# Performance work log

Measured on AMD Instinct MI355X. Metric: run time of the kernel, lower is better.

The kernel has to match this reference:

```python
import jax, jax.numpy as jnp
import numpy as np

N_FREQS = 10
EPS = 1e-5

def embed(p):
    # NeRF positional embedding: [p, sin(p*2^0), cos(p*2^0), ..., sin(p*2^9), cos(p*2^9)]
    freqs = 2.0 ** jnp.arange(N_FREQS, dtype=p.dtype)  # [10]
    ang = p[:, :, None] * freqs[None, None, :]          # [N,3,10]
    sc = jnp.stack([jnp.sin(ang), jnp.cos(ang)], axis=-1)  # [N,3,10,2]
    return jnp.concatenate([p, sc.reshape(p.shape[0], -1)], axis=-1)  # [N, 63]

def edge_conv(x, edge_index, w1, b1, w2, b2):
    src, dst = edge_index[0], edge_index[1]
    xi = x[dst]                                # target features [E, F]
    h = jnp.concatenate([xi, x[src] - xi], -1)  # [E, 2F]
    h = jax.nn.relu(h @ w1 + b1) @ w2 + b2      # [E, out]
    n = x.shape[0]
    s = jax.ops.segment_sum(h, dst, num_segments=n)
    cnt = jax.ops.segment_sum(jnp.ones((h.shape[0],), h.dtype), dst, num_segments=n)
    return s / jnp.clip(cnt, 1.0)[:, None]      # mean aggregation

def batch_norm(x, gamma, beta):
    mu = jnp.mean(x, axis=0)
    var = jnp.mean((x - mu) ** 2, axis=0)
    return (x - mu) * jax.lax.rsqrt(var + EPS) * gamma + beta

def distribute_features(features, face_indices, num_vertices):
    n, f = features.shape
    feat = features.reshape(n * 3, f // 3)
    idx = face_indices.reshape(-1)
    vsum = jax.ops.segment_sum(feat, idx, num_segments=num_vertices)
    cnt = jax.ops.segment_sum(jnp.ones((idx.shape[0],), feat.dtype), idx, num_segments=num_vertices)
    vmean = vsum / jnp.clip(cnt, 1.0)[:, None]
    return vmean[idx].reshape(n, f)

def _mlp_params(key, in_dim, out_dim):
    k1, k2, k3, k4 = jax.random.split(key, 4)
    h = 2 * out_dim
    return (jax.random.normal(k1, (2 * in_dim, h), jnp.float32) * (1.0 / np.sqrt(2 * in_dim)),
            jax.random.normal(k2, (h,), jnp.float32) * 0.01,
            jax.random.normal(k3, (h, out_dim), jnp.float32) * (1.0 / np.sqrt(h)),
            jax.random.normal(k4, (out_dim,), jnp.float32) * 0.01)

def setup_inputs() -> dict:
    key = jax.random.key(0)
    ks = jax.random.split(key, 10)
    N, E, V = 100000, 300000, 50000
    inp = {
        'x': jax.random.normal(ks[0], (N, 16), jnp.float32),
        'edge_index': jax.random.randint(ks[1], (2, E), 0, N, jnp.int32),
        'faces': jax.random.randint(ks[2], (N, 3), 0, V, jnp.int32),
        'num_vertices': V,
    }
    dims = [(196, 96), (96, 192), (192, 384), (384, 384), (384, 576)]
    for i, (di, do) in enumerate(dims, start=1):
        w1, b1, w2, b2 = _mlp_params(ks[2 + i], di, do)
        inp[f'gc{i}_w1'], inp[f'gc{i}_b1'], inp[f'gc{i}_w2'], inp[f'gc{i}_b2'] = w1, b1, w2, b2
    for i, d in enumerate([96, 192, 384, 384], start=1):
        inp[f'gamma{i}'] = jnp.ones((d,), jnp.float32)
        inp[f'beta{i}'] = jnp.zeros((d,), jnp.float32)
    return inp

def reference(x, edge_index, faces, num_vertices,
              gc1_w1, gc1_b1, gc1_w2, gc1_b2,
              gc2_w1, gc2_b1, gc2_w2, gc2_b2,
              gc3_w1, gc3_b1, gc3_w2, gc3_b2,
              gc4_w1, gc4_b1, gc4_w2, gc4_b2,
              gc5_w1, gc5_b1, gc5_w2, gc5_b2,
              gamma1, beta1, gamma2, beta2, gamma3, beta3, gamma4, beta4):
    h = jnp.concatenate([embed(x[:, :3]), embed(x[:, 3:6]), embed(x[:, 6:9]), x[:, 9:]], -1)  # [N,196]
    h = jax.nn.relu(batch_norm(edge_conv(h, edge_index, gc1_w1, gc1_b1, gc1_w2, gc1_b2), gamma1, beta1))
    h = distribute_features(h, faces, num_vertices)
    h = jax.nn.relu(batch_norm(edge_conv(h, edge_index, gc2_w1, gc2_b1, gc2_w2, gc2_b2), gamma2, beta2))
    h = distribute_features(h, faces, num_vertices)
    h = jax.nn.relu(batch_norm(edge_conv(h, edge_index, gc3_w1, gc3_b1, gc3_w2, gc3_b2), gamma3, beta3))
    h = distribute_features(h, faces, num_vertices)
    h = jax.nn.relu(batch_norm(edge_conv(h, edge_index, gc4_w1, gc4_b1, gc4_w2, gc4_b2), gamma4, beta4))
    h = distribute_features(h, faces, num_vertices)
    h = edge_conv(h, edge_index, gc5_w1, gc5_b1, gc5_w2, gc5_b2)
    h = distribute_features(h, faces, num_vertices)
    return h
```

## Files before the change

kernel.cpp:

```cpp
#include <hip/hip_runtime.h>
#include <hip/hip_bf16.h>
#include <stdint.h>


typedef __hip_bfloat16 bf16;
typedef __attribute__((ext_vector_type(8))) short bf16x8;
typedef __attribute__((ext_vector_type(4))) float f32x4;
#define CHUNK 384

static inline int cdiv(int a, int b) { return (a + b - 1) / b; }

__device__ __forceinline__ float bf2f(bf16 v) { return __bfloat162float(v); }
__device__ __forceinline__ bf16 f2bf(float v) { return __float2bfloat16(v); }
__device__ __forceinline__ unsigned short f2bs(float v) {
  bf16 h = __float2bfloat16(v);
  return *reinterpret_cast<unsigned short*>(&h);
}

__device__ __forceinline__ void gload16(const bf16* g, bf16* lds_base) {
  __builtin_amdgcn_global_load_lds((const __attribute__((address_space(1))) void*)g,
                                   (__attribute__((address_space(3))) void*)lds_base,
                                   16, 0, 0);
}

#define WAIT_VM0 asm volatile("s_waitcnt vmcnt(0)" ::: "memory")

__device__ __forceinline__ void swz_decode(int T, int nn, int& mb, int& nb) {
  int i = blockIdx.x;
  int q = T >> 3, r = T & 7;
  int xcd = i & 7, rank = i >> 3;
  int wg = (xcd < r ? xcd * (q + 1) : r * (q + 1) + (xcd - r) * q) + rank;
  nb = wg % nn;
  mb = wg / nn;
}

__global__ __launch_bounds__(256) void k_embed(const float* __restrict__ x,
                                               bf16* __restrict__ h, int N) {
  int idx = blockIdx.x * 256 + threadIdx.x;
  if (idx >= N * 224) return;
  int n = idx / 224;
  int c = idx - n * 224;
  float v = 0.f;
  if (c >= 196) {
    v = 0.f;
  } else if (c >= 189) {
    v = x[n * 16 + 9 + (c - 189)];
  } else {
    int g = c / 63;
    int cc = c - g * 63;
    const float* p = x + n * 16 + g * 3;
    if (cc < 3) {
      v = p[cc];
    } else {
      int t = cc - 3;
      int comp = t / 20;
      int rem = t - comp * 20;
      float ang = p[comp] * (float)(1 << (rem >> 1));
      v = (rem & 1) ? cosf(ang) : sinf(ang);
    }
  }
  h[idx] = f2bf(v);
}

__global__ __launch_bounds__(256) void k_count(const int* __restrict__ idxs,
                                               int* __restrict__ deg, int M) {
  int i = blockIdx.x * 256 + threadIdx.x;
  if (i < M) atomicAdd(&deg[idxs[i]], 1);
}

__global__ __launch_bounds__(256) void k_recip(const int* __restrict__ deg,
                                               float* __restrict__ r, int n) {
  int i = blockIdx.x * 256 + threadIdx.x;
  if (i < n) {
    int d = deg[i];
    r[i] = d > 0 ? 1.f / (float)d : 0.f;
  }
}

__global__ __launch_bounds__(1024) void k_scan(const int* __restrict__ deg,
                                               int* __restrict__ off,
                                               int* __restrict__ cursor, int n) {
  __shared__ int part[1024];
  int t = threadIdx.x;
  int per = (n + 1023) / 1024;
  int b = t * per;
  int e = b + per;
  if (b > n) b = n;
  if (e > n) e = n;
  int s = 0;
  for (int i = b; i < e; ++i) s += deg[i];
  part[t] = s;
  __syncthreads();
  if (t == 0) {
    int r = 0;
    for (int i = 0; i < 1024; ++i) {
      int x = part[i];
      part[i] = r;
      r += x;
    }
    off[n] = r;
  }
  __syncthreads();
  int r = part[t];
  for (int i = b; i < e; ++i) {
    off[i] = r;
    cursor[i] = r;
    r += deg[i];
  }
}

__global__ __launch_bounds__(256) void k_fill_edges(const int* __restrict__ ei, int E,
                                                    int* __restrict__ cursor,
                                                    int* __restrict__ esrc) {
  int e = blockIdx.x * 256 + threadIdx.x;
  if (e >= E) return;
  int dst = ei[E + e];
  int pos = atomicAdd(&cursor[dst], 1);
  esrc[pos] = ei[e];
}

__global__ __launch_bounds__(256) void k_fill_faces(const int* __restrict__ faces, int M,
                                                    int* __restrict__ cursor,
                                                    int* __restrict__ vidx) {
  int i = blockIdx.x * 256 + threadIdx.x;
  if (i >= M) return;
  int v = faces[i];
  int pos = atomicAdd(&cursor[v], 1);
  vidx[pos] = i;
}

__global__ __launch_bounds__(256) void k_prep_w1(const float* __restrict__ w1,
                                                 bf16* __restrict__ WdT,
                                                 bf16* __restrict__ WbT,
                                                 int F, int H, int F_pad, int H_pad) {
  int idx = blockIdx.x * 256 + threadIdx.x;
  if (idx >= H_pad * F_pad) return;
  int n = idx / F_pad;
  int k = idx - n * F_pad;
  float vd = 0.f, vb = 0.f;
  if (n < H && k < F) {
    float top = w1[(size_t)k * H + n];
    float bot = w1[(size_t)(F + k) * H + n];
    vd = top - bot;
    vb = bot;
  }
  WdT[idx] = f2bf(vd);
  WbT[idx] = f2bf(vb);
}

__global__ __launch_bounds__(256) void k_prep_w2(const float* __restrict__ w2,
                                                 bf16* __restrict__ W2T, int H, int O,
                                                 int O_pad) {
  int idx = blockIdx.x * 256 + threadIdx.x;
  if (idx >= O_pad * H) return;
  int n = idx / H;
  int k = idx - n * H;
  float v = (n < O) ? w2[(size_t)k * O + n] : 0.f;
  W2T[idx] = f2bf(v);
}

__global__ __launch_bounds__(256) void gemm1_mfma(
    const bf16* __restrict__ A, int lda,
    const bf16* __restrict__ WdT, const bf16* __restrict__ WbT,
    const float* __restrict__ b1, int c0,
    bf16* __restrict__ outC, bf16* __restrict__ outB,
    int N, int K_pad, int Hc, int nn) {
  __shared__ bf16 sA[2][128 * 32];
  __shared__ bf16 sBd[2][128 * 32];
  __shared__ bf16 sBb[2][128 * 32];
  int mb, nb;
  swz_decode(gridDim.x, nn, mb, nb);
  const int tid = threadIdx.x;
  const int lane = tid & 63, wv = tid >> 6;
  const int wm = wv & 1, wn = wv >> 1;
  const int lr = lane & 15, quad = lane >> 4;
  const int m_blk = mb * 128, n_blk = nb * 128;
  const int rs = lane >> 2;
  const int cg = (lane & 3) ^ ((lane >> 3) & 3);
  const int gsw = (quad ^ ((lr >> 1) & 3)) << 3;
  f32x4 accC[4][4], accB[4][4];
#pragma unroll
  for (int i = 0; i < 4; ++i)
#pragma unroll
    for (int j = 0; j < 4; ++j) {
      accC[i][j] = (f32x4){0.f, 0.f, 0.f, 0.f};
      accB[i][j] = (f32x4){0.f, 0.f, 0.f, 0.f};
    }

  auto stage = [&](int kt, int buf) {
    const int k0 = (kt << 5) + cg * 8;
#pragma unroll
    for (int i = 0; i < 2; ++i) {
      const int rb = wv * 32 + i * 16;
      const int ro = rb + rs;
      gload16(A + (size_t)(m_blk + ro) * lda + k0, &sA[buf][rb * 32]);
      gload16(WdT + (size_t)(n_blk + ro) * K_pad + k0, &sBd[buf][rb * 32]);
      gload16(WbT + (size_t)(n_blk + ro) * K_pad + k0, &sBb[buf][rb * 32]);
    }
  };
  auto compute = [&](int buf) {
    bf16x8 af[4];
#pragma unroll
    for (int im = 0; im < 4; ++im)
      af[im] = *(const bf16x8*)&sA[buf][(wm * 64 + im * 16 + lr) * 32 + gsw];
#pragma unroll
    for (int jn = 0; jn < 4; ++jn) {
      int go = (wn * 64 + jn * 16 + lr) * 32 + gsw;
      bf16x8 bd = *(const bf16x8*)&sBd[buf][go];
      bf16x8 bb = *(const bf16x8*)&sBb[buf][go];
#pragma unroll
      for (int im = 0; im < 4; ++im) {
        accC[im][jn] = __builtin_amdgcn_mfma_f32_16x16x32_bf16(af[im], bd, accC[im][jn], 0, 0, 0);
        accB[im][jn] = __builtin_amdgcn_mfma_f32_16x16x32_bf16(af[im], bb, accB[im][jn], 0, 0, 0);
      }
    }
  };

  const int kTiles = K_pad >> 5;
  stage(0, 0);
  WAIT_VM0;
  __builtin_amdgcn_s_barrier();
  int cur = 0;
  for (int kt = 0; kt < kTiles - 1; ++kt) {
    stage(kt + 1, cur ^ 1);
    compute(cur);
    WAIT_VM0;
    __builtin_amdgcn_s_barrier();
    cur ^= 1;
  }
  compute(cur);

#pragma unroll
  for (int jn = 0; jn < 4; ++jn) {
    int c = n_blk + wn * 64 + jn * 16 + lr;
    if (c >= Hc) continue;
    float bv = b1[c0 + c];
#pragma unroll
    for (int im = 0; im < 4; ++im) {
      int mb2 = m_blk + wm * 64 + im * 16 + quad * 4;
#pragma unroll
      for (int rg = 0; rg < 4; ++rg) {
        int r = mb2 + rg;
        if (r >= N) continue;
        size_t o = (size_t)r * Hc + c;
        outC[o] = f2bf(accC[im][jn][rg] + bv);
        outB[o] = f2bf(accB[im][jn][rg]);
      }
    }
  }
}

__global__ __launch_bounds__(256) void gemm2_mfma(
    const bf16* __restrict__ S, int ldS,
    const bf16* __restrict__ W2T, int ldw,
    const float* __restrict__ b2, const float* __restrict__ rdeg,
    float* __restrict__ Eo, float* __restrict__ stats, int do_stats,
    int N, int K, int O, int nn) {
  __shared__ bf16 sA[2][128 * 32];
  __shared__ bf16 sB[2][128 * 32];
  int mb, nb;
  swz_decode(gridDim.x, nn, mb, nb);
  const int tid = threadIdx.x;
  const int lane = tid & 63, wv = tid >> 6;
  const int wm = wv & 1, wn = wv >> 1;
  const int lr = lane & 15, quad = lane >> 4;
  const int m_blk = mb * 128, n_blk = nb * 128;
  const int rs = lane >> 2;
  const int cg = (lane & 3) ^ ((lane >> 3) & 3);
  const int gsw = (quad ^ ((lr >> 1) & 3)) << 3;
  f32x4 acc[4][4];
#pragma unroll
  for (int i = 0; i < 4; ++i)
#pragma unroll
    for (int j = 0; j < 4; ++j) acc[i][j] = (f32x4){0.f, 0.f, 0.f, 0.f};

  auto stage = [&](int kt, int buf) {
    const int k0 = (kt << 5) + cg * 8;
#pragma unroll
    for (int i = 0; i < 2; ++i) {
      const int rb = wv * 32 + i * 16;
      const int ro = rb + rs;
      gload16(S + (size_t)(m_blk + ro) * ldS + k0, &sA[buf][rb * 32]);
      gload16(W2T + (size_t)(n_blk + ro) * ldw + k0, &sB[buf][rb * 32]);
    }
  };
  auto compute = [&](int buf) {
    bf16x8 af[4];
#pragma unroll
    for (int im = 0; im < 4; ++im)
      af[im] = *(const bf16x8*)&sA[buf][(wm * 64 + im * 16 + lr) * 32 + gsw];
#pragma unroll
    for (int jn = 0; jn < 4; ++jn) {
      bf16x8 bb = *(const bf16x8*)&sB[buf][(wn * 64 + jn * 16 + lr) * 32 + gsw];
#pragma unroll
      for (int im = 0; im < 4; ++im)
        acc[im][jn] = __builtin_amdgcn_mfma_f32_16x16x32_bf16(af[im], bb, acc[im][jn], 0, 0, 0);
    }
  };

  const int kTiles = K >> 5;
  stage(0, 0);
  WAIT_VM0;
  __builtin_amdgcn_s_barrier();
  int cur = 0;
  for (int kt = 0; kt < kTiles - 1; ++kt) {
    stage(kt + 1, cur ^ 1);
    compute(cur);
    WAIT_VM0;
    __builtin_amdgcn_s_barrier();
    cur ^= 1;
  }
  compute(cur);

  float rdv[4][4];
#pragma unroll
  for (int im = 0; im < 4; ++im) {
    int mb2 = m_blk + wm * 64 + im * 16 + quad * 4;
#pragma unroll
    for (int rg = 0; rg < 4; ++rg) {
      int r = mb2 + rg;
      rdv[im][rg] = (r < N) ? rdeg[r] : 0.f;
    }
  }
#pragma unroll
  for (int jn = 0; jn < 4; ++jn) {
    int c = n_blk + wn * 64 + jn * 16 + lr;
    if (c >= O) continue;
    float b2v = b2[c];
    float ssum = 0.f, qsum = 0.f;
#pragma unroll
    for (int im = 0; im < 4; ++im) {
      int mb2 = m_blk + wm * 64 + im * 16 + quad * 4;
#pragma unroll
      for (int rg = 0; rg < 4; ++rg) {
        int r = mb2 + rg;
        if (r >= N) continue;
        float rd = rdv[im][rg];
        float v = acc[im][jn][rg] * rd;
        if (rd != 0.f) v += b2v;
        Eo[(size_t)r * O + c] = v;
        ssum += v;
        qsum += v * v;
      }
    }
    if (do_stats) {
      ssum += __shfl_xor(ssum, 16);
      ssum += __shfl_xor(ssum, 32);
      qsum += __shfl_xor(qsum, 16);
      qsum += __shfl_xor(qsum, 32);
      if (quad == 0) {
        unsafeAtomicAdd(&stats[c], ssum);
        unsafeAtomicAdd(&stats[O + c], qsum);
      }
    }
  }
}

__global__ __launch_bounds__(256) void k_edge_gather(
    const int* __restrict__ eoff, const int* __restrict__ esrc,
    const bf16* __restrict__ C, const bf16* __restrict__ B,
    bf16* __restrict__ S, int ldS, int c0, int N, int Hc) {
  int gw = (blockIdx.x * 256 + threadIdx.x) >> 6;
  int lane = threadIdx.x & 63;
  if (gw >= N) return;
  int beg = eoff[gw], end = eoff[gw + 1];
  const uint32_t* Crow = reinterpret_cast<const uint32_t*>(C + (size_t)gw * Hc);
  float cc0[3], cc1[3], acc0[3], acc1[3];
#pragma unroll
  for (int w = 0; w < 3; ++w) {
    acc0[w] = 0.f;
    acc1[w] = 0.f;
    cc0[w] = 0.f;
    cc1[w] = 0.f;
    int j2 = lane + w * 64;
    if (j2 * 2 < Hc) {
      uint32_t uc = Crow[j2];
      cc0[w] = __uint_as_float(uc << 16);
      cc1[w] = __uint_as_float(uc & 0xffff0000u);
    }
  }
  for (int e = beg; e < end; ++e) {
    int src = esrc[e];
    const uint32_t* Brow = reinterpret_cast<const uint32_t*>(B + (size_t)src * Hc);
#pragma unroll
    for (int w = 0; w < 3; ++w) {
      int j2 = lane + w * 64;
      if (j2 * 2 < Hc) {
        uint32_t ub = Brow[j2];
        acc0[w] += fmaxf(cc0[w] + __uint_as_float(ub << 16), 0.f);
        acc1[w] += fmaxf(cc1[w] + __uint_as_float(ub & 0xffff0000u), 0.f);
      }
    }
  }
  uint32_t* Srow = reinterpret_cast<uint32_t*>(S + (size_t)gw * ldS + c0);
#pragma unroll
  for (int w = 0; w < 3; ++w) {
    int j2 = lane + w * 64;
    if (j2 * 2 < Hc)
      Srow[j2] = ((uint32_t)f2bs(acc1[w]) << 16) | (uint32_t)f2bs(acc0[w]);
  }
}

__global__ __launch_bounds__(256) void k_bn_finalize(const float* __restrict__ stats,
                                                     const float* __restrict__ gamma,
                                                     const float* __restrict__ beta,
                                                     float* __restrict__ scale,
                                                     float* __restrict__ shift, int N, int O) {
  int c = blockIdx.x * 256 + threadIdx.x;
  if (c >= O) return;
  float mu = stats[c] / (float)N;
  float var = stats[O + c] / (float)N - mu * mu;
  float sc = gamma[c] * rsqrtf(var + 1e-5f);
  scale[c] = sc;
  shift[c] = beta[c] - mu * sc;
}

__global__ __launch_bounds__(256) void k_vgather(
    const int* __restrict__ voff, const int* __restrict__ vidx,
    const float* __restrict__ Ef, const float* __restrict__ scale,
    const float* __restrict__ shift, int use_bn,
    float* __restrict__ Vf, int V, int O, int O3) {
  int idx = blockIdx.x * 256 + threadIdx.x;
  if (idx >= V * O3) return;
  int v = idx / O3;
  int c = idx - v * O3;
  int beg = voff[v], end = voff[v + 1];
  float acc = 0.f;
  for (int e = beg; e < end; ++e) {
    int i = vidx[e];
    int n = i / 3;
    int g = i - n * 3;
    int col = g * O3 + c;
    float x = Ef[(size_t)n * O + col];
    if (use_bn) x = fmaxf(fmaf(x, scale[col], shift[col]), 0.f);
    acc += x;
  }
  Vf[idx] = acc;
}

__global__ __launch_bounds__(256) void k_gather_bf16(const float* __restrict__ Vf,
                                                     const int* __restrict__ faces,
                                                     const float* __restrict__ rv,
                                                     bf16* __restrict__ out,
                                                     int N, int O, int O3) {
  int idx = blockIdx.x * 256 + threadIdx.x;
  if (idx >= N * O) return;
  int n = idx / O;
  int c = idx - n * O;
  int g = c / O3;
  int vert = faces[n * 3 + g];
  out[idx] = f2bf(Vf[(size_t)vert * O3 + (c - g * O3)] * rv[vert]);
}

__global__ __launch_bounds__(256) void k_gather_f32(const float* __restrict__ Vf,
                                                    const int* __restrict__ faces,
                                                    const float* __restrict__ rv,
                                                    float* __restrict__ out,
                                                    int N, int O, int O3) {
  int idx = blockIdx.x * 256 + threadIdx.x;
  if (idx >= N * O) return;
  int n = idx / O;
  int c = idx - n * O;
  int g = c / O3;
  int vert = faces[n * 3 + g];
  out[idx] = Vf[(size_t)vert * O3 + (c - g * O3)] * rv[vert];
}

extern "C" void kernel_launch(void* const* d_in, const int* in_sizes, int n_in,
                              void* d_out, int out_size, void* d_ws, size_t ws_size,
                              hipStream_t stream) {
  (void)n_in; (void)out_size; (void)ws_size;
  const float* x = (const float*)d_in[0];
  const int* ei = (const int*)d_in[1];
  const int* faces = (const int*)d_in[2];
  const int N = in_sizes[0] / 16;
  const int E = in_sizes[1] / 2;
  const int V = 50000;
  const int N_pad = cdiv(N, 128) * 128;

  char* p = (char*)d_ws;
  auto carve = [&](size_t bytes) -> char* {
    char* r = p;
    p += (bytes + 255) & ~(size_t)255;
    return r;
  };
  bf16* buf_h = (bf16*)carve((size_t)N_pad * 384 * sizeof(bf16));
  float* buf_e = (float*)carve((size_t)N * 384 * sizeof(float));
  bf16* buf_C = (bf16*)carve((size_t)N * CHUNK * sizeof(bf16));
  bf16* buf_B = (bf16*)carve((size_t)N * CHUNK * sizeof(bf16));
  bf16* buf_S = (bf16*)carve((size_t)N_pad * 1152 * sizeof(bf16));
  float* buf_V = (float*)carve((size_t)V * 192 * sizeof(float));
  bf16* buf_WdT = (bf16*)carve((size_t)1050000 * sizeof(bf16));
  bf16* buf_WbT = (bf16*)carve((size_t)1050000 * sizeof(bf16));
  bf16* buf_W2T = (bf16*)carve((size_t)1500000 * sizeof(bf16));
  int* ideg = (int*)carve((size_t)N * 4);
  int* ivdeg = (int*)carve((size_t)V * 4);
  float* rdegN = (float*)carve((size_t)N * 4);
  float* rdegV = (float*)carve((size_t)V * 4);
  float* stats = (float*)carve(2 * 576 * 4);
  float* scale = (float*)carve(576 * 4);
  float* shift = (float*)carve(576 * 4);
  int* e_off = (int*)carve((size_t)(N + 1) * 4);
  int* e_cur = (int*)carve((size_t)N * 4);
  int* e_src = (int*)carve((size_t)E * 4);
  int* v_off = (int*)carve((size_t)(V + 1) * 4);
  int* v_cur = (int*)carve((size_t)V * 4);
  int* v_idx = (int*)carve((size_t)3 * N * 4);

  hipMemsetAsync(ideg, 0, (size_t)N * 4, stream);
  hipMemsetAsync(ivdeg, 0, (size_t)V * 4, stream);
  k_count<<<cdiv(E, 256), 256, 0, stream>>>(ei + E, ideg, E);
  k_count<<<cdiv(3 * N, 256), 256, 0, stream>>>(faces, ivdeg, 3 * N);
  k_recip<<<cdiv(N, 256), 256, 0, stream>>>(ideg, rdegN, N);
  k_recip<<<cdiv(V, 256), 256, 0, stream>>>(ivdeg, rdegV, V);

  k_scan<<<1, 1024, 0, stream>>>(ideg, e_off, e_cur, N);
  k_scan<<<1, 1024, 0, stream>>>(ivdeg, v_off, v_cur, V);
  k_fill_edges<<<cdiv(E, 256), 256, 0, stream>>>(ei, E, e_cur, e_src);
  k_fill_faces<<<cdiv(3 * N, 256), 256, 0, stream>>>(faces, 3 * N, v_cur, v_idx);

  k_embed<<<cdiv(N * 224, 256), 256, 0, stream>>>(x, buf_h, N);

  const int LF[5] = {196, 96, 192, 384, 384};
  const int LH[5] = {192, 384, 768, 768, 1152};
  const int LO[5] = {96, 192, 384, 384, 576};

  size_t off1 = 0, off2 = 0;
  const int nm = cdiv(N, 128);

  for (int l = 0; l < 5; ++l) {
    const int F = LF[l], H = LH[l], O = LO[l], O3 = O / 3;
    const int F_pad = ((F + 31) / 32) * 32;
    int Hc_last = H % CHUNK;
    if (Hc_last == 0) Hc_last = CHUNK;
    const int H_pad = H - Hc_last + cdiv(Hc_last, 128) * 128;
    const int O_pad = cdiv(O, 128) * 128;
    const float* w1 = (const float*)d_in[4 + l * 4];
    const float* b1 = (const float*)d_in[5 + l * 4];
    const float* w2 = (const float*)d_in[6 + l * 4];
    const float* b2 = (const float*)d_in[7 + l * 4];
    float* Ebuf = (l == 4) ? (float*)d_out : buf_e;
    bf16* WdT = buf_WdT + off1;
    bf16* WbT = buf_WbT + off1;
    bf16* W2T = buf_W2T + off2;
    off1 += (size_t)H_pad * F_pad;
    off2 += (size_t)O_pad * H;

    k_prep_w1<<<cdiv(H_pad * F_pad, 256), 256, 0, stream>>>(w1, WdT, WbT, F, H, F_pad, H_pad);
    k_prep_w2<<<cdiv(O_pad * H, 256), 256, 0, stream>>>(w2, W2T, H, O, O_pad);

    for (int c0 = 0; c0 < H; c0 += CHUNK) {
      int Hc = (H - c0 < CHUNK) ? (H - c0) : CHUNK;
      int nn1 = cdiv(Hc, 128);
      gemm1_mfma<<<nm * nn1, 256, 0, stream>>>(buf_h, F_pad,
                                               WdT + (size_t)c0 * F_pad, WbT + (size_t)c0 * F_pad,
                                               b1, c0, buf_C, buf_B, N, F_pad, Hc, nn1);
      k_edge_gather<<<cdiv(N * 64, 256), 256, 0, stream>>>(e_off, e_src, buf_C, buf_B,
                                                           buf_S, H, c0, N, Hc);
    }

    if (l < 4) hipMemsetAsync(stats, 0, (size_t)2 * O * 4, stream);
    int nn2 = cdiv(O, 128);
    gemm2_mfma<<<nm * nn2, 256, 0, stream>>>(buf_S, H, W2T, H, b2, rdegN, Ebuf,
                                             stats, (l < 4) ? 1 : 0, N, H, O, nn2);

    if (l < 4)
      k_bn_finalize<<<cdiv(O, 256), 256, 0, stream>>>(
          stats, (const float*)d_in[24 + l * 2], (const float*)d_in[25 + l * 2],
          scale, shift, N, O);

    k_vgather<<<cdiv(V * O3, 256), 256, 0, stream>>>(v_off, v_idx, Ebuf, scale, shift,
                                                     (l < 4) ? 1 : 0, buf_V, V, O, O3);
    if (l < 4)
      k_gather_bf16<<<cdiv(N * O, 256), 256, 0, stream>>>(buf_V, faces, rdegV, buf_h, N, O, O3);
    else
      k_gather_f32<<<cdiv(N * O, 256), 256, 0, stream>>>(buf_V, faces, rdegV, (float*)d_out, N, O, O3);
  }
}
```

Before: 4.542 ms.

## Deepen LDS multi-buffering in both MFMA GEMMs with partial vmcnt waits

```diff
diff --git a/kernel.cpp b/kernel.cpp
--- a/kernel.cpp
+++ b/kernel.cpp
@@ -23,7 +23,7 @@
                                    16, 0, 0);
 }
 
-#define WAIT_VM0 asm volatile("s_waitcnt vmcnt(0)" ::: "memory")
+#define WAIT_VM(N) asm volatile("s_waitcnt vmcnt(" #N ")" ::: "memory")
 
 __device__ __forceinline__ void swz_decode(int T, int nn, int& mb, int& nb) {
   int i = blockIdx.x;
@@ -165,9 +165,9 @@
     const float* __restrict__ b1, int c0,
     bf16* __restrict__ outC, bf16* __restrict__ outB,
     int N, int K_pad, int Hc, int nn) {
-  __shared__ bf16 sA[2][128 * 32];
-  __shared__ bf16 sBd[2][128 * 32];
-  __shared__ bf16 sBb[2][128 * 32];
+  __shared__ bf16 sA[3][128 * 32];
+  __shared__ bf16 sBd[3][128 * 32];
+  __shared__ bf16 sBb[3][128 * 32];
   int mb, nb;
   swz_decode(gridDim.x, nn, mb, nb);
   const int tid = threadIdx.x;
@@ -218,17 +218,18 @@
 
   const int kTiles = K_pad >> 5;
   stage(0, 0);
-  WAIT_VM0;
-  __builtin_amdgcn_s_barrier();
-  int cur = 0;
-  for (int kt = 0; kt < kTiles - 1; ++kt) {
-    stage(kt + 1, cur ^ 1);
-    compute(cur);
-    WAIT_VM0;
+  int bt;
+  for (int kt = 0; kt < kTiles; ++kt) {
+    if (kt + 1 < kTiles) {
+      bt = kt + 1;
+      stage(bt, bt - (bt / 3) * 3);
+      WAIT_VM(6);
+    } else {
+      WAIT_VM(0);
+    }
     __builtin_amdgcn_s_barrier();
-    cur ^= 1;
-  }
-  compute(cur);
+    compute(kt - (kt / 3) * 3);
+  }
 
 #pragma unroll
   for (int jn = 0; jn < 4; ++jn) {
@@ -256,8 +257,8 @@
     const float* __restrict__ b2, const float* __restrict__ rdeg,
     float* __restrict__ Eo, float* __restrict__ stats, int do_stats,
     int N, int K, int O, int nn) {
-  __shared__ bf16 sA[2][128 * 32];
-  __shared__ bf16 sB[2][128 * 32];
+  __shared__ bf16 sA[4][128 * 32];
+  __shared__ bf16 sB[4][128 * 32];
   int mb, nb;
   swz_decode(gridDim.x, nn, mb, nb);
   const int tid = threadIdx.x;
@@ -300,17 +301,19 @@
 
   const int kTiles = K >> 5;
   stage(0, 0);
-  WAIT_VM0;
-  __builtin_amdgcn_s_barrier();
-  int cur = 0;
-  for (int kt = 0; kt < kTiles - 1; ++kt) {
-    stage(kt + 1, cur ^ 1);
-    compute(cur);
-    WAIT_VM0;
+  stage(1, 1);
+  for (int kt = 0; kt < kTiles; ++kt) {
+    if (kt + 2 < kTiles) {
+      stage(kt + 2, (kt + 2) & 3);
+      WAIT_VM(8);
+    } else if (kt + 1 < kTiles) {
+      WAIT_VM(4);
+    } else {
+      WAIT_VM(0);
+    }
     __builtin_amdgcn_s_barrier();
-    cur ^= 1;
-  }
-  compute(cur);
+    compute(kt & 3);
+  }
 
   float rdv[4][4];
 #pragma unroll
```

New measurement: 4.834 ms. +6.4%, slower.
